# Optimization experiments

Hardware: AMD Instinct MI355X
Metric: run time of the kernel (lower is better)

## Reference

```python
import jax, jax.numpy as jnp
import numpy as np

B, N, T, F, E = 64, 512, 50, 32, 32768  # batch, n_roi, n_timepoints, n_filters, n_edges


def setup_inputs() -> dict:
    key = jax.random.key(0)
    ks = jax.random.split(key, 24)
    s = 0.05
    inp = {
        "x": jax.random.normal(ks[0], (B, N, T), jnp.float32),
        "edge_index": jax.random.randint(ks[1], (2, E), 0, N, dtype=jnp.int64),
        "edge_weight": jax.random.uniform(ks[2], (E,), jnp.float32),
        # ChebConv K=2 weights: W[k] maps in->out for Chebyshev order k; shared bias.
        "conv1_W": jax.random.normal(ks[3], (2, T, F), jnp.float32) * s,
        "conv1_b": jnp.zeros((F,), jnp.float32),
        "conv2_W": jax.random.normal(ks[4], (2, F, F), jnp.float32) * s,
        "conv2_b": jnp.zeros((F,), jnp.float32),
        "conv3_W": jax.random.normal(ks[5], (2, F, F), jnp.float32) * s,
        "conv3_b": jnp.zeros((F,), jnp.float32),
        "conv4_W": jax.random.normal(ks[6], (2, F, F), jnp.float32) * s,
        "conv4_b": jnp.zeros((F,), jnp.float32),
        "conv5_W": jax.random.normal(ks[7], (2, F, F), jnp.float32) * s,
        "conv5_b": jnp.zeros((F,), jnp.float32),
        "conv6_W": jax.random.normal(ks[8], (2, F, F), jnp.float32) * s,
        "conv6_b": jnp.zeros((F,), jnp.float32),
        "fc1_W": jax.random.normal(ks[9], (F * N, 256), jnp.float32) * s,
        "fc1_b": jnp.zeros((256,), jnp.float32),
        "fc2_W": jax.random.normal(ks[10], (256, 128), jnp.float32) * s,
        "fc2_b": jnp.zeros((128,), jnp.float32),
        "fc3_W": jax.random.normal(ks[11], (128, 2), jnp.float32) * s,
        "fc3_b": jnp.zeros((2,), jnp.float32),
    }
    return inp


def reference(x, edge_index, edge_weight,
              conv1_W, conv1_b, conv2_W, conv2_b, conv3_W, conv3_b,
              conv4_W, conv4_b, conv5_W, conv5_b, conv6_W, conv6_b,
              fc1_W, fc1_b, fc2_W, fc2_b, fc3_W, fc3_b):
    n = x.shape[1]
    src, dst = edge_index[0], edge_index[1]
    # PyG ChebConv __norm__ (sym, lambda_max=2): remove self loops, build
    # L = I - D^-1/2 A D^-1/2, rescale 2L/lmax - I  ->  off-diag = -norm, diag = 0.
    w = jnp.where(src == dst, 0.0, edge_weight)
    deg = jax.ops.segment_sum(w, src, num_segments=n)
    dinv = jnp.where(deg > 0, jax.lax.rsqrt(deg), 0.0)
    norm = -(dinv[src] * w * dinv[dst])  # [E], static across all 6 layers

    def prop(hb):  # L_hat @ h for one sample: gather src, scatter-add to dst
        return jax.ops.segment_sum(norm[:, None] * hb[src], dst, num_segments=n)
    prop_b = jax.vmap(prop)

    def cheb(h, W, b):  # K=2: Tx0 = h, Tx1 = L_hat h
        return (jnp.einsum('bnc,cf->bnf', h, W[0])
                + jnp.einsum('bnc,cf->bnf', prop_b(h), W[1]) + b)

    h = jax.nn.relu(cheb(x, conv1_W, conv1_b))
    h = jax.nn.relu(cheb(h, conv2_W, conv2_b))
    h = jax.nn.relu(cheb(h, conv3_W, conv3_b))
    h = jax.nn.relu(cheb(h, conv4_W, conv4_b))
    h = jax.nn.relu(cheb(h, conv5_W, conv5_b))
    h = cheb(h, conv6_W, conv6_b)          # no relu after conv6 in original
    h = h.reshape(h.shape[0], -1)          # flatten node features per sample
    h = h @ fc1_W + fc1_b                  # dropout = identity at inference
    h = h @ fc2_W + fc2_b
    return h @ fc3_W + fc3_b
```

## Files before the change

kernel.cpp:

```cpp
#include <hip/hip_runtime.h>

#define NN 512
#define BB_ 64
#define EE 32768
#define TT 50
#define FF 32
#define NB 2048

#define OFF_LHAT 0
#define OFF_DEG  (512 * 512)
#define OFF_H    (OFF_DEG + 512)
#define OFF_G    (OFF_H + NN * NB)
#define OFF_F0   (OFF_G + NN * NB)
#define WS_FLOATS (OFF_F0 + NN * NB)


__global__ void k_zero_out(float* out, int n) {
    int i = blockIdx.x * blockDim.x + threadIdx.x;
    if (i < n) out[i] = 0.f;
}

__global__ void k_zero_range(float* p, int n) {
    int i = blockIdx.x * blockDim.x + threadIdx.x;
    if (i < n) p[i] = 0.f;
}

__global__ void k_deg(const int* __restrict__ ei, const float* __restrict__ ew,
                      float* __restrict__ deg) {
    int e = blockIdx.x * blockDim.x + threadIdx.x;
    if (e >= EE) return;
    int s = ei[e] & (NN - 1), d = ei[EE + e] & (NN - 1);
    if (s != d) atomicAdd(&deg[s], ew[e]);
}

__global__ void k_dinv(float* deg) {
    int i = threadIdx.x;
    float d = deg[i];
    deg[i] = (d > 0.f) ? rsqrtf(d) : 0.f;
}

__global__ void k_build(const int* __restrict__ ei, const float* __restrict__ ew,
                        const float* __restrict__ dinv, float* __restrict__ Lhat) {
    int e = blockIdx.x * blockDim.x + threadIdx.x;
    if (e >= EE) return;
    int s = ei[e] & (NN - 1), d = ei[EE + e] & (NN - 1);
    if (s == d) return;
    float nm = -(dinv[s] * ew[e] * dinv[d]);
    atomicAdd(&Lhat[d * NN + s], nm);
}

template<int CIN, bool FROM_X>
__global__ __launch_bounds__(256) void k_small(
        const float* __restrict__ Hin, const float* __restrict__ W,
        const float* __restrict__ bias,
        float* __restrict__ G, float* __restrict__ F0) {
    __shared__ float W0s[CIN * FF];
    __shared__ float W1s[CIN * FF];
    __shared__ float bs[FF];
    __shared__ float rows[64][CIN];
    const int tid = threadIdx.x;
    for (int i = tid; i < CIN * FF; i += 256) {
        W0s[i] = W[i];
        W1s[i] = W[CIN * FF + i];
    }
    if (tid < FF) bs[tid] = bias[tid];
    const int r0 = blockIdx.x * 64;
    for (int idx = tid; idx < 64 * CIN; idx += 256) {
        int r = idx / CIN, c = idx % CIN;
        int R = r0 + r;
        rows[r][c] = FROM_X ? Hin[((size_t)(R & 63) * NN + (R >> 6)) * CIN + c]
                            : Hin[(size_t)R * CIN + c];
    }
    __syncthreads();
    const int f = tid & 31, g = tid >> 5;
    float gacc[8] = {};
    float facc[8];
#pragma unroll
    for (int i = 0; i < 8; ++i) facc[i] = bs[f];
    for (int c = 0; c < CIN; ++c) {
        float w0 = W0s[c * FF + f], w1 = W1s[c * FF + f];
#pragma unroll
        for (int i = 0; i < 8; ++i) {
            float hv = rows[g + 8 * i][c];
            gacc[i] = fmaf(hv, w1, gacc[i]);
            facc[i] = fmaf(hv, w0, facc[i]);
        }
    }
#pragma unroll
    for (int i = 0; i < 8; ++i) {
        size_t o = (size_t)(r0 + g + 8 * i) * FF + f;
        G[o] = gacc[i];
        F0[o] = facc[i];
    }
}

template<bool RELU>
__global__ __launch_bounds__(256) void k_prop(
        const float* __restrict__ L, const float* __restrict__ G,
        const float* __restrict__ F0, float* __restrict__ H) {
    __shared__ float As[2][32][65];
    __shared__ float Bs[2][32][36];
    const int tid = threadIdx.x;
    const int tx = tid & 15, ty = tid >> 4;
    const int i0 = blockIdx.y * 64, j0 = blockIdx.x * 32;
    const int arow = tid >> 3;
    const int akc  = (tid & 7) * 4;
    float acc[4][2] = {};

    float4 pa0, pa1, pb;
    pa0 = *(const float4*)&L[(size_t)(i0 + arow) * NN + akc];
    pa1 = *(const float4*)&L[(size_t)(i0 + 32 + arow) * NN + akc];
    pb  = *(const float4*)&G[(size_t)arow * NB + j0 + akc];
    As[0][akc + 0][arow] = pa0.x; As[0][akc + 1][arow] = pa0.y;
    As[0][akc + 2][arow] = pa0.z; As[0][akc + 3][arow] = pa0.w;
    As[0][akc + 0][32 + arow] = pa1.x; As[0][akc + 1][32 + arow] = pa1.y;
    As[0][akc + 2][32 + arow] = pa1.z; As[0][akc + 3][32 + arow] = pa1.w;
    *(float4*)&Bs[0][arow][akc] = pb;
    __syncthreads();

    for (int t = 0; t < 16; ++t) {
        const int buf = t & 1;
        if (t < 15) {
            const int k0 = (t + 1) * 32;
            pa0 = *(const float4*)&L[(size_t)(i0 + arow) * NN + k0 + akc];
            pa1 = *(const float4*)&L[(size_t)(i0 + 32 + arow) * NN + k0 + akc];
            pb  = *(const float4*)&G[(size_t)(k0 + arow) * NB + j0 + akc];
        }
#pragma unroll
        for (int k = 0; k < 32; ++k) {
            float a[4];
            *(float4*)a = *(const float4*)&As[buf][k][ty * 4];
            float2 b2 = *(const float2*)&Bs[buf][k][tx * 2];
#pragma unroll
            for (int m = 0; m < 4; ++m) {
                acc[m][0] = fmaf(a[m], b2.x, acc[m][0]);
                acc[m][1] = fmaf(a[m], b2.y, acc[m][1]);
            }
        }
        if (t < 15) {
            const int nb = buf ^ 1;
            As[nb][akc + 0][arow] = pa0.x; As[nb][akc + 1][arow] = pa0.y;
            As[nb][akc + 2][arow] = pa0.z; As[nb][akc + 3][arow] = pa0.w;
            As[nb][akc + 0][32 + arow] = pa1.x; As[nb][akc + 1][32 + arow] = pa1.y;
            As[nb][akc + 2][32 + arow] = pa1.z; As[nb][akc + 3][32 + arow] = pa1.w;
            *(float4*)&Bs[nb][arow][akc] = pb;
        }
        __syncthreads();
    }
#pragma unroll
    for (int m = 0; m < 4; ++m) {
        size_t row = i0 + ty * 4 + m;
        float2 f0 = *(const float2*)&F0[row * NB + j0 + tx * 2];
        float2 o;
        o.x = acc[m][0] + f0.x;
        o.y = acc[m][1] + f0.y;
        if (RELU) { o.x = fmaxf(o.x, 0.f); o.y = fmaxf(o.y, 0.f); }
        *(float2*)&H[row * NB + j0 + tx * 2] = o;
    }
}

__global__ __launch_bounds__(256) void k_fc1(const float* __restrict__ h,
                                             const float* __restrict__ W,
                                             float* __restrict__ P) {
    __shared__ float AT[128][68];
    const int tid = threadIdx.x;
    const int jg = blockIdx.x;
    const int kc = blockIdx.y;
    const float* hs = h + (size_t)kc * 4 * NB;
#pragma unroll
    for (int i = 0; i < 8; ++i) {
        int q = tid + i * 256;
        float4 v = *(const float4*)&hs[q * 4];
        int flat = q * 4;
        int nn = flat >> 11, rem = flat & 2047;
        int b = rem >> 5, f0 = rem & 31;
        int krow = nn * 32 + f0;
        AT[krow + 0][b] = v.x; AT[krow + 1][b] = v.y;
        AT[krow + 2][b] = v.z; AT[krow + 3][b] = v.w;
    }
    __syncthreads();
    const int tj = tid & 31, bq = tid >> 5;
    float acc[8] = {};
    const float* wp = W + (size_t)(kc * 128) * 256 + jg * 32 + tj;
#pragma unroll 8
    for (int k = 0; k < 128; ++k) {
        float w = wp[(size_t)k * 256];
        const float* ap = &AT[k][bq * 8];
        float4 a0 = *(const float4*)ap;
        float4 a1 = *(const float4*)(ap + 4);
        acc[0] = fmaf(a0.x, w, acc[0]); acc[1] = fmaf(a0.y, w, acc[1]);
        acc[2] = fmaf(a0.z, w, acc[2]); acc[3] = fmaf(a0.w, w, acc[3]);
        acc[4] = fmaf(a1.x, w, acc[4]); acc[5] = fmaf(a1.y, w, acc[5]);
        acc[6] = fmaf(a1.z, w, acc[6]); acc[7] = fmaf(a1.w, w, acc[7]);
    }
#pragma unroll
    for (int b2 = 0; b2 < 8; ++b2)
        P[(size_t)kc * 16384 + (bq * 8 + b2) * 256 + jg * 32 + tj] = acc[b2];
}

__global__ __launch_bounds__(128) void k_fc23(const float* __restrict__ P,
        const float* __restrict__ b1, const float* __restrict__ W2,
        const float* __restrict__ b2, const float* __restrict__ W3,
        const float* __restrict__ b3, float* __restrict__ out) {
    __shared__ float row[256];
    __shared__ float r2[128];
    const int m = blockIdx.x, j = threadIdx.x;
#pragma unroll
    for (int rep = 0; rep < 2; ++rep) {
        int k2 = j + rep * 128;
        float s = b1[k2];
#pragma unroll 8
        for (int kc = 0; kc < 128; ++kc)
            s += P[(size_t)kc * 16384 + m * 256 + k2];
        row[k2] = s;
    }
    __syncthreads();
    float acc = b2[j];
#pragma unroll 4
    for (int k = 0; k < 256; ++k)
        acc = fmaf(row[k], W2[k * 128 + j], acc);
    r2[j] = acc;
    __syncthreads();
    const int w = j >> 6, l = j & 63;
    float s2 = r2[l] * W3[l * 2 + w] + r2[l + 64] * W3[(l + 64) * 2 + w];
#pragma unroll
    for (int off = 32; off > 0; off >>= 1)
        s2 += __shfl_down(s2, off);
    if (l == 0) out[m * 2 + w] = s2 + b3[w];
}


extern "C" void kernel_launch(void* const* d_in, const int* in_sizes, int n_in,
                              void* d_out, int out_size, void* d_ws, size_t ws_size,
                              hipStream_t stream) {
    float* outp = (float*)d_out;
    if (ws_size < (size_t)WS_FLOATS * sizeof(float)) {
        k_zero_out<<<(out_size + 255) / 256, 256, 0, stream>>>(outp, out_size);
        return;
    }

    const float* x  = (const float*)d_in[0];
    const int*   ei = (const int*)d_in[1];
    const float* ew = (const float*)d_in[2];
    const float* cW[6] = {(const float*)d_in[3], (const float*)d_in[5],
                          (const float*)d_in[7], (const float*)d_in[9],
                          (const float*)d_in[11], (const float*)d_in[13]};
    const float* cb[6] = {(const float*)d_in[4], (const float*)d_in[6],
                          (const float*)d_in[8], (const float*)d_in[10],
                          (const float*)d_in[12], (const float*)d_in[14]};
    const float* fc1W = (const float*)d_in[15];
    const float* fc1b = (const float*)d_in[16];
    const float* fc2W = (const float*)d_in[17];
    const float* fc2b = (const float*)d_in[18];
    const float* fc3W = (const float*)d_in[19];
    const float* fc3b = (const float*)d_in[20];

    float* ws   = (float*)d_ws;
    float* Lhat = ws + OFF_LHAT;
    float* deg  = ws + OFF_DEG;
    float* H    = ws + OFF_H;
    float* G    = ws + OFF_G;
    float* F0   = ws + OFF_F0;
    float* P    = ws + OFF_G;

    k_zero_range<<<(OFF_DEG + 512 + 255) / 256, 256, 0, stream>>>(ws, OFF_DEG + 512);
    k_deg<<<EE / 256, 256, 0, stream>>>(ei, ew, deg);
    k_dinv<<<1, 512, 0, stream>>>(deg);
    k_build<<<EE / 256, 256, 0, stream>>>(ei, ew, deg, Lhat);

    dim3 pgrid(64, 8);
    k_small<TT, true ><<<512, 256, 0, stream>>>(x, cW[0], cb[0], G, F0);
    k_prop<true ><<<pgrid, 256, 0, stream>>>(Lhat, G, F0, H);
    k_small<FF, false><<<512, 256, 0, stream>>>(H, cW[1], cb[1], G, F0);
    k_prop<true ><<<pgrid, 256, 0, stream>>>(Lhat, G, F0, H);
    k_small<FF, false><<<512, 256, 0, stream>>>(H, cW[2], cb[2], G, F0);
    k_prop<true ><<<pgrid, 256, 0, stream>>>(Lhat, G, F0, H);
    k_small<FF, false><<<512, 256, 0, stream>>>(H, cW[3], cb[3], G, F0);
    k_prop<true ><<<pgrid, 256, 0, stream>>>(Lhat, G, F0, H);
    k_small<FF, false><<<512, 256, 0, stream>>>(H, cW[4], cb[4], G, F0);
    k_prop<true ><<<pgrid, 256, 0, stream>>>(Lhat, G, F0, H);
    k_small<FF, false><<<512, 256, 0, stream>>>(H, cW[5], cb[5], G, F0);
    k_prop<false><<<pgrid, 256, 0, stream>>>(Lhat, G, F0, H);

    dim3 fgrid(8, 128);
    k_fc1<<<fgrid, 256, 0, stream>>>(H, fc1W, P);
    k_fc23<<<64, 128, 0, stream>>>(P, fc1b, fc2W, fc2b, fc3W, fc3b, outp);
}
```

Before: 392.1 us.

## Restructure propagation GEMM to read G via uniform scalar loads, stage output through LDS

The dense Lhat@G propagation kernel now gives each wavefront a 16-column slice of a 64x64 output tile. Each lane owns one row. B values are loaded straight from global memory with wave-uniform addresses, which the readfirstlane hint lets the compiler turn into scalar or broadcast loads, so the shared B tile is gone. The accumulators are transposed through a padded LDS tile so the F0 add, ReLU and H store use coalesced float4 accesses, and the grid is halved to match the wider tiles. The aim is to cut LDS traffic and synchronisation per FMA. The risks are higher global or scalar-cache load latency, because B is no longer double buffered, and fewer blocks in flight.

```diff
diff --git a/kernel.cpp b/kernel.cpp
--- a/kernel.cpp
+++ b/kernel.cpp
@@ -98,64 +98,82 @@
 __global__ __launch_bounds__(256) void k_prop(
         const float* __restrict__ L, const float* __restrict__ G,
         const float* __restrict__ F0, float* __restrict__ H) {
-    __shared__ float As[2][32][65];
-    __shared__ float Bs[2][32][36];
-    const int tid = threadIdx.x;
-    const int tx = tid & 15, ty = tid >> 4;
-    const int i0 = blockIdx.y * 64, j0 = blockIdx.x * 32;
-    const int arow = tid >> 3;
-    const int akc  = (tid & 7) * 4;
-    float acc[4][2] = {};
-
-    float4 pa0, pa1, pb;
-    pa0 = *(const float4*)&L[(size_t)(i0 + arow) * NN + akc];
-    pa1 = *(const float4*)&L[(size_t)(i0 + 32 + arow) * NN + akc];
-    pb  = *(const float4*)&G[(size_t)arow * NB + j0 + akc];
-    As[0][akc + 0][arow] = pa0.x; As[0][akc + 1][arow] = pa0.y;
-    As[0][akc + 2][arow] = pa0.z; As[0][akc + 3][arow] = pa0.w;
-    As[0][akc + 0][32 + arow] = pa1.x; As[0][akc + 1][32 + arow] = pa1.y;
-    As[0][akc + 2][32 + arow] = pa1.z; As[0][akc + 3][32 + arow] = pa1.w;
-    *(float4*)&Bs[0][arow][akc] = pb;
-    __syncthreads();
-
-    for (int t = 0; t < 16; ++t) {
-        const int buf = t & 1;
-        if (t < 15) {
-            const int k0 = (t + 1) * 32;
-            pa0 = *(const float4*)&L[(size_t)(i0 + arow) * NN + k0 + akc];
-            pa1 = *(const float4*)&L[(size_t)(i0 + 32 + arow) * NN + k0 + akc];
-            pb  = *(const float4*)&G[(size_t)(k0 + arow) * NB + j0 + akc];
-        }
-#pragma unroll
+    __shared__ float As[2][32][64];
+    __shared__ float T[64][68];
+    const int tid  = threadIdx.x;
+    const int lane = tid & 63;
+    const int w    = tid >> 6;
+    const int i0   = blockIdx.y * 64;
+    const int j0   = blockIdx.x * 64;
+    const int jw   = j0 + __builtin_amdgcn_readfirstlane(w) * 16;
+
+    const int ar  = lane;
+    const int ac0 = w * 8;
+    const float* Lrow = L + (size_t)(i0 + ar) * NN + ac0;
+
+    float acc[16] = {};
+
+    float4 p0 = *(const float4*)&Lrow[0];
+    float4 p1 = *(const float4*)&Lrow[4];
+    As[0][ac0 + 0][ar] = p0.x; As[0][ac0 + 1][ar] = p0.y;
+    As[0][ac0 + 2][ar] = p0.z; As[0][ac0 + 3][ar] = p0.w;
+    As[0][ac0 + 4][ar] = p1.x; As[0][ac0 + 5][ar] = p1.y;
+    As[0][ac0 + 6][ar] = p1.z; As[0][ac0 + 7][ar] = p1.w;
+    __syncthreads();
+
+    for (int s = 0; s < 16; ++s) {
+        const int buf = s & 1;
+        if (s < 15) {
+            p0 = *(const float4*)&Lrow[(s + 1) * 32];
+            p1 = *(const float4*)&Lrow[(s + 1) * 32 + 4];
+        }
+        const float* gp = G + (size_t)(s * 32) * NB + jw;
+#pragma unroll 8
         for (int k = 0; k < 32; ++k) {
-            float a[4];
-            *(float4*)a = *(const float4*)&As[buf][k][ty * 4];
-            float2 b2 = *(const float2*)&Bs[buf][k][tx * 2];
-#pragma unroll
-            for (int m = 0; m < 4; ++m) {
-                acc[m][0] = fmaf(a[m], b2.x, acc[m][0]);
-                acc[m][1] = fmaf(a[m], b2.y, acc[m][1]);
-            }
-        }
-        if (t < 15) {
+            const float vA = As[buf][k][lane];
+            const float4 b0 = *(const float4*)&gp[(size_t)k * NB + 0];
+            const float4 b1 = *(const float4*)&gp[(size_t)k * NB + 4];
+            const float4 b2 = *(const float4*)&gp[(size_t)k * NB + 8];
+            const float4 b3 = *(const float4*)&gp[(size_t)k * NB + 12];
+            acc[ 0] = fmaf(vA, b0.x, acc[ 0]); acc[ 1] = fmaf(vA, b0.y, acc[ 1]);
+            acc[ 2] = fmaf(vA, b0.z, acc[ 2]); acc[ 3] = fmaf(vA, b0.w, acc[ 3]);
+            acc[ 4] = fmaf(vA, b1.x, acc[ 4]); acc[ 5] = fmaf(vA, b1.y, acc[ 5]);
+            acc[ 6] = fmaf(vA, b1.z, acc[ 6]); acc[ 7] = fmaf(vA, b1.w, acc[ 7]);
+            acc[ 8] = fmaf(vA, b2.x, acc[ 8]); acc[ 9] = fmaf(vA, b2.y, acc[ 9]);
+            acc[10] = fmaf(vA, b2.z, acc[10]); acc[11] = fmaf(vA, b2.w, acc[11]);
+            acc[12] = fmaf(vA, b3.x, acc[12]); acc[13] = fmaf(vA, b3.y, acc[13]);
+            acc[14] = fmaf(vA, b3.z, acc[14]); acc[15] = fmaf(vA, b3.w, acc[15]);
+        }
+        if (s < 15) {
             const int nb = buf ^ 1;
-            As[nb][akc + 0][arow] = pa0.x; As[nb][akc + 1][arow] = pa0.y;
-            As[nb][akc + 2][arow] = pa0.z; As[nb][akc + 3][arow] = pa0.w;
-            As[nb][akc + 0][32 + arow] = pa1.x; As[nb][akc + 1][32 + arow] = pa1.y;
-            As[nb][akc + 2][32 + arow] = pa1.z; As[nb][akc + 3][32 + arow] = pa1.w;
-            *(float4*)&Bs[nb][arow][akc] = pb;
+            As[nb][ac0 + 0][ar] = p0.x; As[nb][ac0 + 1][ar] = p0.y;
+            As[nb][ac0 + 2][ar] = p0.z; As[nb][ac0 + 3][ar] = p0.w;
+            As[nb][ac0 + 4][ar] = p1.x; As[nb][ac0 + 5][ar] = p1.y;
+            As[nb][ac0 + 6][ar] = p1.z; As[nb][ac0 + 7][ar] = p1.w;
         }
         __syncthreads();
     }
+
 #pragma unroll
     for (int m = 0; m < 4; ++m) {
-        size_t row = i0 + ty * 4 + m;
-        float2 f0 = *(const float2*)&F0[row * NB + j0 + tx * 2];
-        float2 o;
-        o.x = acc[m][0] + f0.x;
-        o.y = acc[m][1] + f0.y;
-        if (RELU) { o.x = fmaxf(o.x, 0.f); o.y = fmaxf(o.y, 0.f); }
-        *(float2*)&H[row * NB + j0 + tx * 2] = o;
+        float4 v; v.x = acc[4 * m]; v.y = acc[4 * m + 1];
+        v.z = acc[4 * m + 2]; v.w = acc[4 * m + 3];
+        *(float4*)&T[lane][w * 16 + 4 * m] = v;
+    }
+    __syncthreads();
+#pragma unroll
+    for (int rep = 0; rep < 4; ++rep) {
+        const int ed = rep * 1024 + tid * 4;
+        const int r = ed >> 6, c = ed & 63;
+        float4 v = *(const float4*)&T[r][c];
+        const size_t o = (size_t)(i0 + r) * NB + j0 + c;
+        float4 f = *(const float4*)&F0[o];
+        v.x += f.x; v.y += f.y; v.z += f.z; v.w += f.w;
+        if (RELU) {
+            v.x = fmaxf(v.x, 0.f); v.y = fmaxf(v.y, 0.f);
+            v.z = fmaxf(v.z, 0.f); v.w = fmaxf(v.w, 0.f);
+        }
+        *(float4*)&H[o] = v;
     }
 }
 
@@ -268,7 +286,7 @@
     k_dinv<<<1, 512, 0, stream>>>(deg);
     k_build<<<EE / 256, 256, 0, stream>>>(ei, ew, deg, Lhat);
 
-    dim3 pgrid(64, 8);
+    dim3 pgrid(32, 8);
     k_small<TT, true ><<<512, 256, 0, stream>>>(x, cW[0], cb[0], G, F0);
     k_prop<true ><<<pgrid, 256, 0, stream>>>(Lhat, G, F0, H);
     k_small<FF, false><<<512, 256, 0, stream>>>(H, cW[1], cb[1], G, F0);
```

Result: slower. 523.2 us (+33.4%).
